# Kernel optimization log

Measured on AMD Instinct MI355X. Metric: run time of the kernel, lower is better.

## Reference

```python
import jax, jax.numpy as jnp
import numpy as np
from jax.scipy.linalg import solve_triangular

B, T, HID = 1, 2048, 2048
HK, DK = 16, 96
HV, DV = 16, 192
KDIM, VDIM = HK * DK, HV * DV
KCONV = 4
CHUNK = 64
EPS = 1e-6


def setup_inputs():
    key = jax.random.key(0)
    ks = jax.random.split(key, 16)
    s = 0.02
    return {
        "hidden_states": jax.random.normal(ks[0], (B, T, HID), jnp.float32),
        "Wq": jax.random.normal(ks[1], (HID, KDIM), jnp.float32) * s,
        "Wk": jax.random.normal(ks[2], (HID, KDIM), jnp.float32) * s,
        "Wv": jax.random.normal(ks[3], (HID, VDIM), jnp.float32) * s,
        "Wb": jax.random.normal(ks[4], (HID, HV), jnp.float32) * s,
        "Wa": jax.random.normal(ks[5], (HID, HV), jnp.float32) * s,
        "Wg": jax.random.normal(ks[6], (HID, VDIM), jnp.float32) * s,
        "Wo": jax.random.normal(ks[7], (VDIM, HID), jnp.float32) * s,
        "conv_q": jax.random.normal(ks[8], (KDIM, KCONV), jnp.float32) * 0.5,
        "conv_k": jax.random.normal(ks[9], (KDIM, KCONV), jnp.float32) * 0.5,
        "conv_v": jax.random.normal(ks[10], (VDIM, KCONV), jnp.float32) * 0.5,
        "A_log": jnp.log(jax.random.uniform(ks[11], (HV,), jnp.float32, 1.0, 16.0)),
        "dt_bias": jax.random.uniform(ks[12], (HV,), jnp.float32, 0.0, 1.0),
        "norm_weight": jnp.ones((DV,), jnp.float32),
    }


def short_conv_silu(x, w):
    # x: [B,T,C], w: [C,K]; causal depthwise conv (left pad K-1) then SiLU
    K = w.shape[-1]
    xp = jnp.pad(x, ((0, 0), (K - 1, 0), (0, 0)))
    y = sum(xp[:, j:j + x.shape[1], :] * w[:, j] for j in range(K))
    return jax.nn.silu(y)


def l2norm(x):
    return x * jax.lax.rsqrt(jnp.sum(x * x, axis=-1, keepdims=True) + EPS)


def chunk_gated_delta_rule(q, k, v, g, beta):
    # q,k: [B,T,H,dk]; v: [B,T,H,dv]; g,beta: [B,T,H]. Chunked parallel scan (WY form).
    Bb, Tt, H, dk = q.shape
    dv = v.shape[-1]
    N = Tt // CHUNK
    q = l2norm(q) * (dk ** -0.5)
    k = l2norm(k)
    chunk = lambda x: x.transpose(0, 2, 1, 3).reshape(Bb, H, N, CHUNK, x.shape[-1])
    qc, kc, vc = chunk(q), chunk(k), chunk(v)
    gc = jnp.cumsum(g.transpose(0, 2, 1).reshape(Bb, H, N, CHUNK), axis=-1)
    bc = beta.transpose(0, 2, 1).reshape(Bb, H, N, CHUNK)

    m_inc = jnp.tril(jnp.ones((CHUNK, CHUNK), bool))
    m_str = jnp.tril(jnp.ones((CHUNK, CHUNK), bool), -1)
    diff = gc[..., :, None] - gc[..., None, :]
    D = jnp.exp(jnp.where(m_inc, diff, 0.0)) * m_inc  # [B,H,N,C,C] intra-chunk decay

    kb = kc * bc[..., None]
    A = -jnp.einsum('bhnik,bhnjk->bhnij', kb, kc) * D * m_str
    eye = jnp.eye(CHUNK, dtype=q.dtype)
    # UT transform: Tm = (I - A)^{-1}, A strictly lower triangular
    Tm = solve_triangular(eye - A, jnp.broadcast_to(eye, A.shape), lower=True, unit_diagonal=True)
    u = Tm @ (vc * bc[..., None])                   # [B,H,N,C,dv]
    w = Tm @ (kb * jnp.exp(gc)[..., None])          # [B,H,N,C,dk]
    g_last = gc[..., -1]                            # [B,H,N]

    def step(S, inp):
        q_i, k_i, u_i, w_i, g_i, D_i, gl = inp
        v_new = u_i - w_i @ S                       # [B,H,C,dv]
        attn = jnp.einsum('bhik,bhjk->bhij', q_i, k_i) * D_i
        o_i = (q_i * jnp.exp(g_i)[..., None]) @ S + attn @ v_new
        k_dec = k_i * jnp.exp(gl[..., None] - g_i)[..., None]
        S = S * jnp.exp(gl)[..., None, None] + jnp.einsum('bhck,bhcv->bhkv', k_dec, v_new)
        return S, o_i

    mv = lambda x: jnp.moveaxis(x, 2, 0)
    S0 = jnp.zeros((Bb, H, dk, dv), q.dtype)
    _, o = jax.lax.scan(step, S0, (mv(qc), mv(kc), mv(u), mv(w), mv(gc), mv(D), mv(g_last)))
    o = jnp.moveaxis(o, 0, 2).reshape(Bb, H, Tt, dv)
    return o.transpose(0, 2, 1, 3)                  # [B,T,H,dv]


def reference(hidden_states, Wq, Wk, Wv, Wb, Wa, Wg, Wo, conv_q, conv_k, conv_v, A_log, dt_bias, norm_weight):
    q = short_conv_silu(hidden_states @ Wq, conv_q).reshape(B, T, HK, DK)
    k = short_conv_silu(hidden_states @ Wk, conv_k).reshape(B, T, HK, DK)
    v = short_conv_silu(hidden_states @ Wv, conv_v).reshape(B, T, HV, DV)
    beta = jax.nn.sigmoid(hidden_states @ Wb) * 2.0          # allow_neg_eigval -> beta in [0,2]
    g = -jnp.exp(A_log) * jax.nn.softplus(hidden_states @ Wa + dt_bias)  # log decay, [B,T,HV]
    o = chunk_gated_delta_rule(q, k, v, g, beta)             # [B,T,HV,DV]
    gate = (hidden_states @ Wg).reshape(B, T, HV, DV)
    o = o * jax.nn.silu(gate)                                # gated RMSNorm (gate, then norm)
    o = o * jax.lax.rsqrt(jnp.mean(o * o, axis=-1, keepdims=True) + EPS) * norm_weight
    return o.reshape(B, T, VDIM) @ Wo
```

## Files before the change

### kernel.cpp

```cpp
#include <hip/hip_runtime.h>
#include <math.h>

#define T_LEN 2048
#define HIDN  2048
#define HKN   16
#define DKN   96
#define HVN   16
#define DVN   192
#define KDIMN 1536
#define VDIMN 3072
#define QKVD  6144
#define CHUNKN 64
#define NCHUNK 32
#define EPSF 1e-6f
#define TN_STRIDE 10240
#define WQG_ST 6656
#define AT_ST  4608
#define CT_ST  18432
#define S_ST   19968
#define U_ST   12288

typedef __attribute__((ext_vector_type(8))) short short8;
typedef __attribute__((ext_vector_type(4))) float f32x4;

__device__ __forceinline__ unsigned short f2bf(float f) {
    unsigned int u = __float_as_uint(f);
    unsigned int r = (u + 0x7FFFu + ((u >> 16) & 1u)) >> 16;
    return (unsigned short)r;
}
__device__ __forceinline__ float bf2f(unsigned short u) {
    return __uint_as_float(((unsigned int)u) << 16);
}
__device__ __forceinline__ float siluf(float x) { return x / (1.f + expf(-x)); }

__device__ __forceinline__ void gld_lds16(const void* g, void* l) {
    __builtin_amdgcn_global_load_lds((const __attribute__((address_space(1))) unsigned int*)g,
                                     (__attribute__((address_space(3))) unsigned int*)l, 16, 0, 0);
}

__global__ void prep_weights(const float* __restrict__ Wq, const float* __restrict__ Wk,
                             const float* __restrict__ Wv, const float* __restrict__ Wg,
                             const float* __restrict__ Wo,
                             unsigned short* __restrict__ WallT, unsigned short* __restrict__ WoT) {
    __shared__ float tile[64][65];
    int bid = blockIdx.x;
    const float* W; unsigned short* Wt; int K, N, l;
    if (bid < 768)       { W = Wq; Wt = WallT;                          K = 2048; N = 1536; l = bid; }
    else if (bid < 1536) { W = Wk; Wt = WallT + (size_t)1536 * 2048;    K = 2048; N = 1536; l = bid - 768; }
    else if (bid < 3072) { W = Wv; Wt = WallT + (size_t)3072 * 2048;    K = 2048; N = 3072; l = bid - 1536; }
    else if (bid < 4608) { W = Wg; Wt = WallT + (size_t)6144 * 2048;    K = 2048; N = 3072; l = bid - 3072; }
    else                 { W = Wo; Wt = WoT;                            K = 3072; N = 2048; l = bid - 4608; }
    int nbx = N >> 6;
    int n0 = (l % nbx) * 64, k0 = (l / nbx) * 64;
    int tx = threadIdx.x, ty = threadIdx.y;
    for (int r = ty; r < 64; r += 4) tile[r][tx] = W[(size_t)(k0 + r) * N + n0 + tx];
    __syncthreads();
    for (int r = ty; r < 64; r += 4) Wt[(size_t)(n0 + r) * K + k0 + tx] = f2bf(tile[tx][r]);
}

__global__ __launch_bounds__(256) void gemm_bt2(const unsigned short* __restrict__ A,
                                                const unsigned short* __restrict__ Bt,
                                                float* __restrict__ C1, int ld1, int nblk1,
                                                unsigned short* __restrict__ C2, int ld2,
                                                int M, int K) {
    __shared__ __align__(16) unsigned short As[2][128 * 32];
    __shared__ __align__(16) unsigned short Bs[2][128 * 32];
    int tid = threadIdx.x;
    int wave = tid >> 6, lane = tid & 63;
    int bm = blockIdx.y, bn = blockIdx.x;
    f32x4 acc[4][4] = {};
    int wr = wave >> 1, wc = wave & 1;
    int rstage = wave * 32 + (lane >> 2);
    int cstage = (lane & 3) * 8;
    const size_t a_row0 = (size_t)bm * 128;
    const size_t b_row0 = (size_t)bn * 128;
    const unsigned short* gaBase = A + (a_row0 + rstage) * (size_t)K + cstage;
    const unsigned short* gbBase = Bt + (b_row0 + rstage) * (size_t)K + cstage;
    int row_a[4], row_b[4];
#pragma unroll
    for (int i = 0; i < 4; ++i) {
        row_a[i] = wr * 64 + i * 16 + (lane & 15);
        row_b[i] = wc * 64 + i * 16 + (lane & 15);
    }
    int koff = (lane >> 4) * 8;
    int niter = K >> 5;
    {
        unsigned short* ab = &As[0][wave * 1024];
        unsigned short* bb = &Bs[0][wave * 1024];
        gld_lds16(gaBase, ab);
        gld_lds16(gaBase + (size_t)16 * K, ab + 512);
        gld_lds16(gbBase, bb);
        gld_lds16(gbBase + (size_t)16 * K, bb + 512);
    }
    __syncthreads();
    for (int i = 0; i < niter; ++i) {
        int cur = i & 1;
        if (i + 1 < niter) {
            int k0 = (i + 1) * 32;
            unsigned short* ab = &As[cur ^ 1][wave * 1024];
            unsigned short* bb = &Bs[cur ^ 1][wave * 1024];
            gld_lds16(gaBase + k0, ab);
            gld_lds16(gaBase + k0 + (size_t)16 * K, ab + 512);
            gld_lds16(gbBase + k0, bb);
            gld_lds16(gbBase + k0 + (size_t)16 * K, bb + 512);
        }
        short8 af[4], bfr[4];
#pragma unroll
        for (int mi = 0; mi < 4; ++mi) af[mi] = *(const short8*)&As[cur][row_a[mi] * 32 + koff];
#pragma unroll
        for (int ni = 0; ni < 4; ++ni) bfr[ni] = *(const short8*)&Bs[cur][row_b[ni] * 32 + koff];
#pragma unroll
        for (int mi = 0; mi < 4; ++mi)
#pragma unroll
            for (int ni = 0; ni < 4; ++ni)
                acc[mi][ni] = __builtin_amdgcn_mfma_f32_16x16x32_bf16(af[mi], bfr[ni], acc[mi][ni], 0, 0, 0);
        __syncthreads();
    }
    if (bn < nblk1) {
        int colb = bn * 128;
#pragma unroll
        for (int mi = 0; mi < 4; ++mi) {
            int rbase = bm * 128 + wr * 64 + mi * 16 + (lane >> 4) * 4;
#pragma unroll
            for (int ni = 0; ni < 4; ++ni) {
                int col = colb + wc * 64 + ni * 16 + (lane & 15);
#pragma unroll
                for (int j = 0; j < 4; ++j)
                    C1[(size_t)(rbase + j) * ld1 + col] = acc[mi][ni][j];
            }
        }
    } else {
        int colb = (bn - nblk1) * 128;
#pragma unroll
        for (int mi = 0; mi < 4; ++mi) {
            int rbase = bm * 128 + wr * 64 + mi * 16 + (lane >> 4) * 4;
#pragma unroll
            for (int ni = 0; ni < 4; ++ni) {
                int col = colb + wc * 64 + ni * 16 + (lane & 15);
#pragma unroll
                for (int j = 0; j < 4; ++j)
                    C2[(size_t)(rbase + j) * ld2 + col] = f2bf(acc[mi][ni][j]);
            }
        }
    }
}

__global__ __launch_bounds__(256) void gemm_btk(const unsigned short* __restrict__ A,
                                                const unsigned short* __restrict__ Bt,
                                                float* __restrict__ C, float* __restrict__ Cp,
                                                int M, int N, int K) {
    __shared__ __align__(16) unsigned short As[2][128 * 32];
    __shared__ __align__(16) unsigned short Bs[2][128 * 32];
    int tid = threadIdx.x;
    int wave = tid >> 6, lane = tid & 63;
    int bm = blockIdx.y, bn = blockIdx.x, kz = blockIdx.z;
    int kchunk = K / 3;
    int kbeg = kz * kchunk;
    f32x4 acc[4][4] = {};
    int wr = wave >> 1, wc = wave & 1;
    int rstage = wave * 32 + (lane >> 2);
    int cstage = (lane & 3) * 8;
    const size_t a_row0 = (size_t)bm * 128;
    const size_t b_row0 = (size_t)bn * 128;
    const unsigned short* gaBase = A + (a_row0 + rstage) * (size_t)K + kbeg + cstage;
    const unsigned short* gbBase = Bt + (b_row0 + rstage) * (size_t)K + kbeg + cstage;
    int row_a[4], row_b[4];
#pragma unroll
    for (int i = 0; i < 4; ++i) {
        row_a[i] = wr * 64 + i * 16 + (lane & 15);
        row_b[i] = wc * 64 + i * 16 + (lane & 15);
    }
    int koff = (lane >> 4) * 8;
    int niter = kchunk >> 5;
    {
        unsigned short* ab = &As[0][wave * 1024];
        unsigned short* bb = &Bs[0][wave * 1024];
        gld_lds16(gaBase, ab);
        gld_lds16(gaBase + (size_t)16 * K, ab + 512);
        gld_lds16(gbBase, bb);
        gld_lds16(gbBase + (size_t)16 * K, bb + 512);
    }
    __syncthreads();
    for (int i = 0; i < niter; ++i) {
        int cur = i & 1;
        if (i + 1 < niter) {
            int k0 = (i + 1) * 32;
            unsigned short* ab = &As[cur ^ 1][wave * 1024];
            unsigned short* bb = &Bs[cur ^ 1][wave * 1024];
            gld_lds16(gaBase + k0, ab);
            gld_lds16(gaBase + k0 + (size_t)16 * K, ab + 512);
            gld_lds16(gbBase + k0, bb);
            gld_lds16(gbBase + k0 + (size_t)16 * K, bb + 512);
        }
        short8 af[4], bfr[4];
#pragma unroll
        for (int mi = 0; mi < 4; ++mi) af[mi] = *(const short8*)&As[cur][row_a[mi] * 32 + koff];
#pragma unroll
        for (int ni = 0; ni < 4; ++ni) bfr[ni] = *(const short8*)&Bs[cur][row_b[ni] * 32 + koff];
#pragma unroll
        for (int mi = 0; mi < 4; ++mi)
#pragma unroll
            for (int ni = 0; ni < 4; ++ni)
                acc[mi][ni] = __builtin_amdgcn_mfma_f32_16x16x32_bf16(af[mi], bfr[ni], acc[mi][ni], 0, 0, 0);
        __syncthreads();
    }
    float* Cout = (kz == 0) ? C : (Cp + (size_t)(kz - 1) * M * N);
#pragma unroll
    for (int mi = 0; mi < 4; ++mi) {
        int rbase = bm * 128 + wr * 64 + mi * 16 + (lane >> 4) * 4;
#pragma unroll
        for (int ni = 0; ni < 4; ++ni) {
            int col = bn * 128 + wc * 64 + ni * 16 + (lane & 15);
#pragma unroll
            for (int j = 0; j < 4; ++j)
                Cout[(size_t)(rbase + j) * N + col] = acc[mi][ni][j];
        }
    }
}

__global__ void addk(float* __restrict__ out, const float* __restrict__ p, int n) {
    int i = (blockIdx.x * blockDim.x + threadIdx.x) * 4;
    if (i >= n) return;
    float4 a = *(const float4*)(out + i);
    float4 b = *(const float4*)(p + i);
    float4 c = *(const float4*)(p + n + i);
    a.x += b.x + c.x; a.y += b.y + c.y; a.z += b.z + c.z; a.w += b.w + c.w;
    *(float4*)(out + i) = a;
}

__global__ __launch_bounds__(256) void beta_g(const float* __restrict__ X,
                                              const float* __restrict__ Wb, const float* __restrict__ Wa,
                                              const float* __restrict__ A_log, const float* __restrict__ dtb,
                                              float* __restrict__ bvec, float* __restrict__ gvec,
                                              unsigned short* __restrict__ Xbf) {
    int t = blockIdx.x;
    int tid = threadIdx.x;
    int cg = tid & 7, ks = tid >> 3;
    int wave = tid >> 6, lane = tid & 63;
    const float* xr = X + (size_t)t * HIDN;
    const float* Wsel = (cg < 4) ? Wb : Wa;
    int cc = (cg & 3) * 4;
    float ax = 0.f, ay = 0.f, az = 0.f, aw = 0.f;
#pragma unroll 4
    for (int i = 0; i < 16; ++i) {
        int k = (ks + 32 * i) * 4;
        float4 xv = *(const float4*)(xr + k);
        if (cg == 0) {
            ushort4 xo;
            xo.x = f2bf(xv.x); xo.y = f2bf(xv.y); xo.z = f2bf(xv.z); xo.w = f2bf(xv.w);
            *(ushort4*)(Xbf + (size_t)t * HIDN + k) = xo;
        }
        float4 w0 = *(const float4*)(Wsel + (size_t)(k + 0) * 16 + cc);
        float4 w1 = *(const float4*)(Wsel + (size_t)(k + 1) * 16 + cc);
        float4 w2 = *(const float4*)(Wsel + (size_t)(k + 2) * 16 + cc);
        float4 w3 = *(const float4*)(Wsel + (size_t)(k + 3) * 16 + cc);
        ax += xv.x * w0.x + xv.y * w1.x + xv.z * w2.x + xv.w * w3.x;
        ay += xv.x * w0.y + xv.y * w1.y + xv.z * w2.y + xv.w * w3.y;
        az += xv.x * w0.z + xv.y * w1.z + xv.z * w2.z + xv.w * w3.z;
        aw += xv.x * w0.w + xv.y * w1.w + xv.z * w2.w + xv.w * w3.w;
    }
#pragma unroll
    for (int off = 8; off <= 32; off <<= 1) {
        ax += __shfl_xor(ax, off, 64);
        ay += __shfl_xor(ay, off, 64);
        az += __shfl_xor(az, off, 64);
        aw += __shfl_xor(aw, off, 64);
    }
    __shared__ float red[4][8][4];
    if ((lane >> 3) == 0) {
        red[wave][cg][0] = ax; red[wave][cg][1] = ay;
        red[wave][cg][2] = az; red[wave][cg][3] = aw;
    }
    __syncthreads();
    if (tid < 8) {
        float tot[4];
#pragma unroll
        for (int j = 0; j < 4; ++j)
            tot[j] = red[0][tid][j] + red[1][tid][j] + red[2][tid][j] + red[3][tid][j];
        int c0 = (tid & 3) * 4;
        if (tid < 4) {
#pragma unroll
            for (int j = 0; j < 4; ++j)
                bvec[(size_t)t * 16 + c0 + j] = 2.f / (1.f + expf(-tot[j]));
        } else {
#pragma unroll
            for (int j = 0; j < 4; ++j) {
                float a = tot[j] + dtb[c0 + j];
                float sp = (a > 20.f) ? a : log1pf(expf(a));
                gvec[(size_t)t * 16 + c0 + j] = -expf(A_log[c0 + j]) * sp;
            }
        }
    }
}

__global__ __launch_bounds__(256) void phase1_mfma(
    const float* __restrict__ Cqkv,
    const float* __restrict__ cq, const float* __restrict__ ck, const float* __restrict__ cv,
    const float* __restrict__ gvec, const float* __restrict__ bvec,
    float* __restrict__ u_ws, unsigned short* __restrict__ w_bf,
    unsigned short* __restrict__ qg_bf, unsigned short* __restrict__ at_bf,
    unsigned short* __restrict__ Ct, unsigned short* __restrict__ Tn) {
    int n = blockIdx.x, h = blockIdx.y;
    int t0 = n * CHUNKN;
    int tid = threadIdx.x;
    int wave = tid >> 6, lane = tid & 63;
    size_t base = (size_t)(h * NCHUNK + n);

    __shared__ __align__(16) char LB1[139776];
    unsigned short* QKb  = (unsigned short*)(LB1 + 0);
    unsigned short* Pb   = (unsigned short*)(LB1 + 26624);
    unsigned short* RHSw = (unsigned short*)(LB1 + 39936);
    unsigned short* RHSv = (unsigned short*)(LB1 + 53760);
    unsigned short* Ab   = (unsigned short*)(LB1 + 81408);
    unsigned short* Atb  = (unsigned short*)(LB1 + 94720);
    unsigned short* Ptb  = (unsigned short*)(LB1 + 108032);
    float*          Pf   = (float*)(LB1 + 121344);
    unsigned short* kdT  = (unsigned short*)(LB1 + 81408);
    unsigned short* wT   = (unsigned short*)(LB1 + 95232);
    unsigned short* uT   = (unsigned short*)(LB1 + 109056);
    float* gr_s = (float*)(LB1 + 138752);
    float* gc_s = gr_s + 64;
    float* be_s = gc_s + 64;
    float* egc  = be_s + 64;
    __shared__ __align__(16) float cwS[384 * 4];

    for (int f = tid; f < 384; f += 256) {
        const float* src = (f < 96)  ? (cq + (size_t)(h * 96 + f) * 4)
                         : (f < 192) ? (ck + (size_t)(h * 96 + f - 96) * 4)
                                     : (cv + (size_t)(h * 192 + f - 192) * 4);
        *(float4*)&cwS[f * 4] = *(const float4*)src;
    }
    if (tid < 64) {
        gr_s[tid] = gvec[(size_t)(t0 + tid) * HVN + h];
        be_s[tid] = bvec[(size_t)(t0 + tid) * HVN + h];
    }
    __syncthreads();
    if (tid < 64) {
        float sacc = 0.f;
        for (int j = 0; j <= tid; ++j) sacc += gr_s[j];
        gc_s[tid] = sacc;
    }
    __syncthreads();
    float gl = gc_s[63];
    if (tid < 64) egc[tid] = expf(gl - gc_s[tid]);

    int r = tid >> 2, sub = tid & 3;
    int trow = t0 + r;
    {
        int gc0 = 1536 + h * DKN + sub * 24;
        int lc0 = 96 + sub * 24;
        float kreg[24];
        float ss = 0.f;
#pragma unroll
        for (int i = 0; i < 6; ++i) {
            float4 x0 = (trow >= 3) ? *(const float4*)(Cqkv + (size_t)(trow - 3) * QKVD + gc0 + i * 4) : make_float4(0, 0, 0, 0);
            float4 x1 = (trow >= 2) ? *(const float4*)(Cqkv + (size_t)(trow - 2) * QKVD + gc0 + i * 4) : make_float4(0, 0, 0, 0);
            float4 x2 = (trow >= 1) ? *(const float4*)(Cqkv + (size_t)(trow - 1) * QKVD + gc0 + i * 4) : make_float4(0, 0, 0, 0);
            float4 x3 = *(const float4*)(Cqkv + (size_t)trow * QKVD + gc0 + i * 4);
#pragma unroll
            for (int c = 0; c < 4; ++c) {
                float4 w = *(const float4*)&cwS[(lc0 + i * 4 + c) * 4];
                float xv = ((const float*)&x0)[c] * w.x + ((const float*)&x1)[c] * w.y
                         + ((const float*)&x2)[c] * w.z + ((const float*)&x3)[c] * w.w;
                xv = siluf(xv);
                kreg[i * 4 + c] = xv;
                ss += xv * xv;
            }
        }
        ss += __shfl_xor(ss, 1, 64);
        ss += __shfl_xor(ss, 2, 64);
        float nrm = rsqrtf(ss + EPSF);
        float ebg = be_s[r] * expf(gc_s[r]);
#pragma unroll
        for (int i = 0; i < 24; ++i) {
            float kn = kreg[i] * nrm;
            QKb[r * 104 + sub * 24 + i] = f2bf(kn);
            RHSw[(sub * 24 + i) * 72 + r] = f2bf(kn * ebg);
        }
    }
    {
        int gc0 = h * DKN + sub * 24;
        int lc0 = sub * 24;
        float qreg[24];
        float ss = 0.f;
#pragma unroll
        for (int i = 0; i < 6; ++i) {
            float4 x0 = (trow >= 3) ? *(const float4*)(Cqkv + (size_t)(trow - 3) * QKVD + gc0 + i * 4) : make_float4(0, 0, 0, 0);
            float4 x1 = (trow >= 2) ? *(const float4*)(Cqkv + (size_t)(trow - 2) * QKVD + gc0 + i * 4) : make_float4(0, 0, 0, 0);
            float4 x2 = (trow >= 1) ? *(const float4*)(Cqkv + (size_t)(trow - 1) * QKVD + gc0 + i * 4) : make_float4(0, 0, 0, 0);
            float4 x3 = *(const float4*)(Cqkv + (size_t)trow * QKVD + gc0 + i * 4);
#pragma unroll
            for (int c = 0; c < 4; ++c) {
                float4 w = *(const float4*)&cwS[(lc0 + i * 4 + c) * 4];
                float xv = ((const float*)&x0)[c] * w.x + ((const float*)&x1)[c] * w.y
                         + ((const float*)&x2)[c] * w.z + ((const float*)&x3)[c] * w.w;
                xv = siluf(xv);
                qreg[i * 4 + c] = xv;
                ss += xv * xv;
            }
        }
        ss += __shfl_xor(ss, 1, 64);
        ss += __shfl_xor(ss, 2, 64);
        float nrm = rsqrtf(ss + EPSF) * 0.10206207261596577f;
        float eg = expf(gc_s[r]);
        unsigned short* qgp = qg_bf + base * WQG_ST + r * 104 + sub * 24;
#pragma unroll
        for (int i = 0; i < 24; ++i) {
            float qn = qreg[i] * nrm;
            QKb[(64 + r) * 104 + sub * 24 + i] = f2bf(qn);
            qgp[i] = f2bf(qn * eg);
        }
    }
    {
        int gc0 = 3072 + h * DVN + sub * 48;
        int lc0 = 192 + sub * 48;
        float ber = be_s[r];
#pragma unroll
        for (int i = 0; i < 12; ++i) {
            float4 x0 = (trow >= 3) ? *(const float4*)(Cqkv + (size_t)(trow - 3) * QKVD + gc0 + i * 4) : make_float4(0, 0, 0, 0);
            float4 x1 = (trow >= 2) ? *(const float4*)(Cqkv + (size_t)(trow - 2) * QKVD + gc0 + i * 4) : make_float4(0, 0, 0, 0);
            float4 x2 = (trow >= 1) ? *(const float4*)(Cqkv + (size_t)(trow - 1) * QKVD + gc0 + i * 4) : make_float4(0, 0, 0, 0);
            float4 x3 = *(const float4*)(Cqkv + (size_t)trow * QKVD + gc0 + i * 4);
#pragma unroll
            for (int c = 0; c < 4; ++c) {
                float4 w = *(const float4*)&cwS[(lc0 + i * 4 + c) * 4];
                float xv = ((const float*)&x0)[c] * w.x + ((const float*)&x1)[c] * w.y
                         + ((const float*)&x2)[c] * w.z + ((const float*)&x3)[c] * w.w;
                RHSv[(sub * 48 + i * 4 + c) * 72 + r] = f2bf(siluf(xv) * ber);
            }
        }
    }
    __syncthreads();

    {
        f32x4 acc1[2][4] = {};
#pragma unroll
        for (int ks = 0; ks < 3; ++ks) {
            int ko = ks * 32 + (lane >> 4) * 8;
            short8 af[2], bfv[4];
#pragma unroll
            for (int rt2 = 0; rt2 < 2; ++rt2)
                af[rt2] = *(const short8*)&QKb[(wave * 32 + rt2 * 16 + (lane & 15)) * 104 + ko];
#pragma unroll
            for (int ct = 0; ct < 4; ++ct)
                bfv[ct] = *(const short8*)&QKb[(ct * 16 + (lane & 15)) * 104 + ko];
#pragma unroll
            for (int rt2 = 0; rt2 < 2; ++rt2)
#pragma unroll
                for (int ct = 0; ct < 4; ++ct)
                    acc1[rt2][ct] = __builtin_amdgcn_mfma_f32_16x16x32_bf16(af[rt2], bfv[ct], acc1[rt2][ct], 0, 0, 0);
        }
#pragma unroll
        for (int rt2 = 0; rt2 < 2; ++rt2)
#pragma unroll
            for (int ct = 0; ct < 4; ++ct)
#pragma unroll
                for (int j = 0; j < 4; ++j) {
                    int rr = wave * 32 + rt2 * 16 + (lane >> 4) * 4 + j;
                    int cc = ct * 16 + (lane & 15);
                    float val = acc1[rt2][ct][j];
                    if (rr < 64) {
                        float av = (rr > cc) ? -be_s[rr] * expf(gc_s[rr] - gc_s[cc]) * val : 0.f;
                        unsigned short ab = f2bf(av);
                        Ab[rr * 104 + cc] = ab;
                        Atb[cc * 104 + rr] = ab;
                        float pv = (rr == cc) ? 1.f : av;
                        Pf[rr * 68 + cc] = pv;
                        unsigned short pb = f2bf(pv);
                        Pb[rr * 104 + cc] = pb;
                        Ptb[cc * 104 + rr] = pb;
                    } else {
                        int ar = rr - 64;
                        float av = (ar >= cc) ? expf(gc_s[ar] - gc_s[cc]) * val : 0.f;
                        at_bf[base * AT_ST + ar * 72 + cc] = f2bf(av);
                    }
                }
    }
    __syncthreads();

#pragma unroll 1
    for (int lev = 0; lev < 5; ++lev) {
        f32x4 d[4] = {};
#pragma unroll
        for (int ks = 0; ks < 2; ++ks) {
            int ko = ks * 32 + (lane >> 4) * 8;
            short8 a0 = *(const short8*)&Ab[(wave * 16 + (lane & 15)) * 104 + ko];
#pragma unroll
            for (int ct = 0; ct < 4; ++ct) {
                short8 b0 = *(const short8*)&Atb[(ct * 16 + (lane & 15)) * 104 + ko];
                d[ct] = __builtin_amdgcn_mfma_f32_16x16x32_bf16(a0, b0, d[ct], 0, 0, 0);
            }
        }
        __syncthreads();
#pragma unroll
        for (int ct = 0; ct < 4; ++ct)
#pragma unroll
            for (int j = 0; j < 4; ++j) {
                int rr = wave * 16 + (lane >> 4) * 4 + j;
                int cc = ct * 16 + (lane & 15);
                unsigned short hb = f2bf(d[ct][j]);
                Ab[rr * 104 + cc] = hb;
                Atb[cc * 104 + rr] = hb;
            }
        __syncthreads();
        f32x4 e[4];
#pragma unroll
        for (int ct = 0; ct < 4; ++ct)
#pragma unroll
            for (int j = 0; j < 4; ++j)
                e[ct][j] = Pf[(wave * 16 + (lane >> 4) * 4 + j) * 68 + ct * 16 + (lane & 15)];
#pragma unroll
        for (int ks = 0; ks < 2; ++ks) {
            int ko = ks * 32 + (lane >> 4) * 8;
            short8 a0 = *(const short8*)&Ab[(wave * 16 + (lane & 15)) * 104 + ko];
#pragma unroll
            for (int ct = 0; ct < 4; ++ct) {
                short8 b0 = *(const short8*)&Ptb[(ct * 16 + (lane & 15)) * 104 + ko];
                e[ct] = __builtin_amdgcn_mfma_f32_16x16x32_bf16(a0, b0, e[ct], 0, 0, 0);
            }
        }
        __syncthreads();
#pragma unroll
        for (int ct = 0; ct < 4; ++ct)
#pragma unroll
            for (int j = 0; j < 4; ++j) {
                int rr = wave * 16 + (lane >> 4) * 4 + j;
                int cc = ct * 16 + (lane & 15);
                float pv = e[ct][j];
                Pf[rr * 68 + cc] = pv;
                unsigned short pb = f2bf(pv);
                Pb[rr * 104 + cc] = pb;
                Ptb[cc * 104 + rr] = pb;
            }
        __syncthreads();
    }
    for (int f = tid; f < 6144; f += 256) {
        int d = f >> 6, tt = f & 63;
        kdT[d * 72 + tt] = f2bf(bf2f(QKb[tt * 104 + d]) * egc[tt]);
    }

#pragma unroll 1
    for (int i = 0; i < 18; ++i) {
        int id = wave * 18 + i;
        int rt = id & 3, ct = id >> 2;
        f32x4 o4 = {};
#pragma unroll
        for (int ks = 0; ks < 2; ++ks) {
            int ko = ks * 32 + (lane >> 4) * 8;
            short8 a0 = *(const short8*)&Pb[(rt * 16 + (lane & 15)) * 104 + ko];
            short8 b0 = (ct < 12)
                ? *(const short8*)&RHSv[(ct * 16 + (lane & 15)) * 72 + ko]
                : *(const short8*)&RHSw[((ct - 12) * 16 + (lane & 15)) * 72 + ko];
            o4 = __builtin_amdgcn_mfma_f32_16x16x32_bf16(a0, b0, o4, 0, 0, 0);
        }
#pragma unroll
        for (int j = 0; j < 4; ++j) {
            int rr = rt * 16 + (lane >> 4) * 4 + j;
            int nn = ct * 16 + (lane & 15);
            if (ct < 12) {
                u_ws[base * U_ST + rr * 192 + nn] = o4[j];
                uT[nn * 72 + rr] = f2bf(o4[j]);
            } else {
                w_bf[base * WQG_ST + rr * 104 + (nn - 192)] = f2bf(-o4[j]);
                wT[(nn - 192) * 72 + rr] = f2bf(o4[j]);
            }
        }
    }
    __syncthreads();

    float eglv = expf(gl);
#pragma unroll 1
    for (int q = 0; q < 27; ++q) {
        int id = wave * 27 + q;
        f32x4 acc = {};
        if (id < 36) {
            int jt = id / 6, kt = id % 6;
#pragma unroll
            for (int ks = 0; ks < 2; ++ks) {
                int ko = ks * 32 + (lane >> 4) * 8;
                short8 a0 = *(const short8*)&kdT[(jt * 16 + (lane & 15)) * 72 + ko];
                short8 b0 = *(const short8*)&wT[(kt * 16 + (lane & 15)) * 72 + ko];
                acc = __builtin_amdgcn_mfma_f32_16x16x32_bf16(a0, b0, acc, 0, 0, 0);
            }
#pragma unroll
            for (int rr = 0; rr < 4; ++rr) {
                int j = jt * 16 + (lane >> 4) * 4 + rr;
                int k = kt * 16 + (lane & 15);
                float val = -acc[rr];
                if (j == k) val += eglv;
                Tn[base * TN_STRIDE + j * 104 + k] = f2bf(val);
            }
        } else {
            int cid = id - 36;
            int it = cid / 6, jt = cid % 6;
#pragma unroll
            for (int ks = 0; ks < 2; ++ks) {
                int ko = ks * 32 + (lane >> 4) * 8;
                short8 a0 = *(const short8*)&uT[(it * 16 + (lane & 15)) * 72 + ko];
                short8 b0 = *(const short8*)&kdT[(jt * 16 + (lane & 15)) * 72 + ko];
                acc = __builtin_amdgcn_mfma_f32_16x16x32_bf16(a0, b0, acc, 0, 0, 0);
            }
#pragma unroll
            for (int rr = 0; rr < 4; ++rr)
                Ct[base * CT_ST + (size_t)(it * 16 + (lane >> 4) * 4 + rr) * 96 + jt * 16 + (lane & 15)] = f2bf(acc[rr]);
        }
    }
}

__global__ __launch_bounds__(128) void mscan(const unsigned short* __restrict__ Ct,
                                             const unsigned short* __restrict__ Tn,
                                             unsigned short* __restrict__ s_bf) {
    int rg = blockIdx.x, h = blockIdx.y;
    int tid = threadIdx.x, wave = tid >> 6, lane = tid & 63;
    __shared__ __align__(16) unsigned short St[48 * 104];
    __shared__ __align__(16) unsigned short TnB[2][TN_STRIDE];
// ... 208 lines not shown
        for (int m = 0; m < 48; ++m) {
            int i = qq * 48 + m;
            float x = oF[i * 68 + jj];
            float g = bf2f(gp[m]);
            float xv = x * siluf(g);
            oF[i * 68 + jj] = xv;
            ss += xv * xv;
        }
        ssq[jj * 4 + qq] = ss;
    }
    __syncthreads();
    if (tid < 64) {
        float tot = ssq[tid * 4] + ssq[tid * 4 + 1] + ssq[tid * 4 + 2] + ssq[tid * 4 + 3];
        rno[tid] = rsqrtf(tot * (1.f / 192.f) + EPSF);
    }
    __syncthreads();
    {
        float rr2 = rno[jj];
        unsigned short* op = obf + (size_t)(t0 + jj) * VDIMN + h * DVN + qq * 48;
#pragma unroll 4
        for (int m = 0; m < 48; ++m) {
            int i = qq * 48 + m;
            op[m] = f2bf(oF[i * 68 + jj] * rr2 * nw[i]);
        }
    }
}

extern "C" void kernel_launch(void* const* d_in, const int* in_sizes, int n_in,
                              void* d_out, int out_size, void* d_ws, size_t ws_size,
                              hipStream_t stream) {
    (void)in_sizes; (void)n_in; (void)out_size;
    const float* X    = (const float*)d_in[0];
    const float* Wq   = (const float*)d_in[1];
    const float* Wk   = (const float*)d_in[2];
    const float* Wv   = (const float*)d_in[3];
    const float* Wb   = (const float*)d_in[4];
    const float* Wa   = (const float*)d_in[5];
    const float* Wg   = (const float*)d_in[6];
    const float* Wo   = (const float*)d_in[7];
    const float* cq   = (const float*)d_in[8];
    const float* ck   = (const float*)d_in[9];
    const float* cv   = (const float*)d_in[10];
    const float* Alog = (const float*)d_in[11];
    const float* dtb  = (const float*)d_in[12];
    const float* nw   = (const float*)d_in[13];

    const size_t OFF_XBF   = 0;
    const size_t OFF_WALLT = 8388608;
    const size_t OFF_WOT   = 46137344;
    const size_t OFF_CQKV  = 58720256;
    const size_t OFF_CGATE = 109051904;
    const size_t OFF_CT    = 134217728;
    const size_t OFF_TN    = OFF_CT + 37748736;
    const size_t OFF_GVEC  = 184549376;
    const size_t OFF_BVEC  = 184680448;
    const size_t OFF_U     = 184819712;
    const size_t OFF_W     = 209985536;
    const size_t OFF_QG    = 222568448;
    const size_t OFF_AT    = OFF_XBF;
    const size_t OFF_S     = OFF_CQKV;
    const size_t OFF_OBF   = OFF_WALLT + 25165824;
    const size_t OFF_OPART = OFF_CQKV;
    const size_t NEEDED    = 235151360;
    if (ws_size < NEEDED) return;

    char* ws = (char*)d_ws;
    unsigned short* Xbf   = (unsigned short*)(ws + OFF_XBF);
    unsigned short* WallT = (unsigned short*)(ws + OFF_WALLT);
    unsigned short* WoT   = (unsigned short*)(ws + OFF_WOT);
    float* Cqkv  = (float*)(ws + OFF_CQKV);
    unsigned short* Cgate = (unsigned short*)(ws + OFF_CGATE);
    float* gvec  = (float*)(ws + OFF_GVEC);
    float* bvec  = (float*)(ws + OFF_BVEC);
    float* u_ws  = (float*)(ws + OFF_U);
    unsigned short* w_bf  = (unsigned short*)(ws + OFF_W);
    unsigned short* qg_bf = (unsigned short*)(ws + OFF_QG);
    unsigned short* at_bf = (unsigned short*)(ws + OFF_AT);
    unsigned short* Ct    = (unsigned short*)(ws + OFF_CT);
    unsigned short* Tn    = (unsigned short*)(ws + OFF_TN);
    unsigned short* s_bf  = (unsigned short*)(ws + OFF_S);
    unsigned short* obf   = (unsigned short*)(ws + OFF_OBF);
    float* opart = (float*)(ws + OFF_OPART);

    beta_g<<<T_LEN, 256, 0, stream>>>(X, Wb, Wa, Alog, dtb, bvec, gvec, Xbf);
    prep_weights<<<6144, dim3(64, 4), 0, stream>>>(Wq, Wk, Wv, Wg, Wo, WallT, WoT);

    gemm_bt2<<<dim3(9216 / 128, 2048 / 128), 256, 0, stream>>>(Xbf, WallT,
                                                               Cqkv, QKVD, QKVD / 128,
                                                               Cgate, VDIMN, 2048, 2048);

    phase1_mfma<<<dim3(NCHUNK, HVN), 256, 0, stream>>>(Cqkv, cq, ck, cv, gvec, bvec,
                                                       u_ws, w_bf, qg_bf, at_bf, Ct, Tn);
    mscan<<<dim3(4, HVN), 128, 0, stream>>>(Ct, Tn, s_bf);
    phase2b_mfma<<<dim3(NCHUNK, HVN), 256, 0, stream>>>(s_bf, w_bf, qg_bf, at_bf, u_ws,
                                                        Cgate, nw, obf);

    gemm_btk<<<dim3(2048 / 128, 2048 / 128, 3), 256, 0, stream>>>(obf, WoT, (float*)d_out, opart,
                                                                  2048, 2048, 3072);
    addk<<<4096, 256, 0, stream>>>((float*)d_out, opart, 2048 * 2048);
}
```

Baseline: 402.7 us.

## Deepen GEMM K-tiles with swizzled LDS, merge prep kernels, restructure inverse doubling

```diff
diff --git a/kernel.cpp b/kernel.cpp
--- a/kernel.cpp
+++ b/kernel.cpp
@@ -38,24 +38,106 @@
                                      (__attribute__((address_space(3))) unsigned int*)l, 16, 0, 0);
 }
 
-__global__ void prep_weights(const float* __restrict__ Wq, const float* __restrict__ Wk,
-                             const float* __restrict__ Wv, const float* __restrict__ Wg,
-                             const float* __restrict__ Wo,
-                             unsigned short* __restrict__ WallT, unsigned short* __restrict__ WoT) {
+__device__ __forceinline__ void stage_tile64(const unsigned short* __restrict__ G,
+                                             size_t row0, int K, int kt,
+                                             unsigned short* lds, int wave, int lane) {
+#pragma unroll
+    for (int q = 0; q < 4; ++q) {
+        int c = q * 4 + wave;
+        int row = c * 8 + (lane >> 3);
+        int col = ((lane & 7) ^ (lane >> 3)) * 8;
+        gld_lds16(G + (row0 + row) * (size_t)K + kt + col, (char*)lds + c * 1024);
+    }
+}
+__device__ __forceinline__ short8 lds_read_swz(const unsigned short* lds, int row, int kbyte) {
+    return *(const short8*)((const char*)lds + row * 128 + (kbyte ^ ((row & 7) << 4)));
+}
+
+__global__ __launch_bounds__(256) void prep_all(
+    const float* __restrict__ X,
+    const float* __restrict__ Wb, const float* __restrict__ Wa,
+    const float* __restrict__ A_log, const float* __restrict__ dtb,
+    float* __restrict__ bvec, float* __restrict__ gvec, unsigned short* __restrict__ Xbf,
+    const float* __restrict__ Wq, const float* __restrict__ Wk,
+    const float* __restrict__ Wv, const float* __restrict__ Wg,
+    const float* __restrict__ Wo,
+    unsigned short* __restrict__ WallT, unsigned short* __restrict__ WoT) {
     __shared__ float tile[64][65];
+    __shared__ float red[4][8][4];
     int bid = blockIdx.x;
-    const float* W; unsigned short* Wt; int K, N, l;
-    if (bid < 768)       { W = Wq; Wt = WallT;                          K = 2048; N = 1536; l = bid; }
-    else if (bid < 1536) { W = Wk; Wt = WallT + (size_t)1536 * 2048;    K = 2048; N = 1536; l = bid - 768; }
-    else if (bid < 3072) { W = Wv; Wt = WallT + (size_t)3072 * 2048;    K = 2048; N = 3072; l = bid - 1536; }
-    else if (bid < 4608) { W = Wg; Wt = WallT + (size_t)6144 * 2048;    K = 2048; N = 3072; l = bid - 3072; }
-    else                 { W = Wo; Wt = WoT;                            K = 3072; N = 2048; l = bid - 4608; }
-    int nbx = N >> 6;
-    int n0 = (l % nbx) * 64, k0 = (l / nbx) * 64;
-    int tx = threadIdx.x, ty = threadIdx.y;
-    for (int r = ty; r < 64; r += 4) tile[r][tx] = W[(size_t)(k0 + r) * N + n0 + tx];
-    __syncthreads();
-    for (int r = ty; r < 64; r += 4) Wt[(size_t)(n0 + r) * K + k0 + tx] = f2bf(tile[tx][r]);
+    int tid = threadIdx.x;
+    if (bid < 2048) {
+        int t = bid;
+        int cg = tid & 7, ks = tid >> 3;
+        int wave = tid >> 6, lane = tid & 63;
+        const float* xr = X + (size_t)t * HIDN;
+        const float* Wsel = (cg < 4) ? Wb : Wa;
+        int cc = (cg & 3) * 4;
+        float ax = 0.f, ay = 0.f, az = 0.f, aw = 0.f;
+#pragma unroll 4
+        for (int i = 0; i < 16; ++i) {
+            int k = (ks + 32 * i) * 4;
+            float4 xv = *(const float4*)(xr + k);
+            if (cg == 0) {
+                ushort4 xo;
+                xo.x = f2bf(xv.x); xo.y = f2bf(xv.y); xo.z = f2bf(xv.z); xo.w = f2bf(xv.w);
+                *(ushort4*)(Xbf + (size_t)t * HIDN + k) = xo;
+            }
+            float4 w0 = *(const float4*)(Wsel + (size_t)(k + 0) * 16 + cc);
+            float4 w1 = *(const float4*)(Wsel + (size_t)(k + 1) * 16 + cc);
+            float4 w2 = *(const float4*)(Wsel + (size_t)(k + 2) * 16 + cc);
+            float4 w3 = *(const float4*)(Wsel + (size_t)(k + 3) * 16 + cc);
+            ax += xv.x * w0.x + xv.y * w1.x + xv.z * w2.x + xv.w * w3.x;
+            ay += xv.x * w0.y + xv.y * w1.y + xv.z * w2.y + xv.w * w3.y;
+            az += xv.x * w0.z + xv.y * w1.z + xv.z * w2.z + xv.w * w3.z;
+            aw += xv.x * w0.w + xv.y * w1.w + xv.z * w2.w + xv.w * w3.w;
+        }
+#pragma unroll
+        for (int off = 8; off <= 32; off <<= 1) {
+            ax += __shfl_xor(ax, off, 64);
+            ay += __shfl_xor(ay, off, 64);
+            az += __shfl_xor(az, off, 64);
+            aw += __shfl_xor(aw, off, 64);
+        }
+        if ((lane >> 3) == 0) {
+            red[wave][cg][0] = ax; red[wave][cg][1] = ay;
+            red[wave][cg][2] = az; red[wave][cg][3] = aw;
+        }
+        __syncthreads();
+        if (tid < 8) {
+            float tot[4];
+#pragma unroll
+            for (int j = 0; j < 4; ++j)
+                tot[j] = red[0][tid][j] + red[1][tid][j] + red[2][tid][j] + red[3][tid][j];
+            int c0 = (tid & 3) * 4;
+            if (tid < 4) {
+#pragma unroll
+                for (int j = 0; j < 4; ++j)
+                    bvec[(size_t)t * 16 + c0 + j] = 2.f / (1.f + expf(-tot[j]));
+            } else {
+#pragma unroll
+                for (int j = 0; j < 4; ++j) {
+                    float a = tot[j] + dtb[c0 + j];
+                    float sp = (a > 20.f) ? a : log1pf(expf(a));
+                    gvec[(size_t)t * 16 + c0 + j] = -expf(A_log[c0 + j]) * sp;
+                }
+            }
+        }
+    } else {
+        int b2 = bid - 2048;
+        const float* W; unsigned short* Wt; int K, N, l;
+        if (b2 < 768)       { W = Wq; Wt = WallT;                       K = 2048; N = 1536; l = b2; }
+        else if (b2 < 1536) { W = Wk; Wt = WallT + (size_t)1536 * 2048; K = 2048; N = 1536; l = b2 - 768; }
+        else if (b2 < 3072) { W = Wv; Wt = WallT + (size_t)3072 * 2048; K = 2048; N = 3072; l = b2 - 1536; }
+        else if (b2 < 4608) { W = Wg; Wt = WallT + (size_t)6144 * 2048; K = 2048; N = 3072; l = b2 - 3072; }
+        else                { W = Wo; Wt = WoT;                         K = 3072; N = 2048; l = b2 - 4608; }
+        int nbx = N >> 6;
+        int n0 = (l % nbx) * 64, k0 = (l / nbx) * 64;
+        int tx = tid & 63, ty = tid >> 6;
+        for (int r = ty; r < 64; r += 4) tile[r][tx] = W[(size_t)(k0 + r) * N + n0 + tx];
+        __syncthreads();
+        for (int r = ty; r < 64; r += 4) Wt[(size_t)(n0 + r) * K + k0 + tx] = f2bf(tile[tx][r]);
+    }
 }
 
 __global__ __launch_bounds__(256) void gemm_bt2(const unsigned short* __restrict__ A,
@@ -63,57 +145,45 @@
                                                 float* __restrict__ C1, int ld1, int nblk1,
                                                 unsigned short* __restrict__ C2, int ld2,
                                                 int M, int K) {
-    __shared__ __align__(16) unsigned short As[2][128 * 32];
-    __shared__ __align__(16) unsigned short Bs[2][128 * 32];
+    __shared__ __align__(16) unsigned short As[2][128 * 64];
+    __shared__ __align__(16) unsigned short Bs[2][128 * 64];
     int tid = threadIdx.x;
     int wave = tid >> 6, lane = tid & 63;
     int bm = blockIdx.y, bn = blockIdx.x;
     f32x4 acc[4][4] = {};
     int wr = wave >> 1, wc = wave & 1;
-    int rstage = wave * 32 + (lane >> 2);
-    int cstage = (lane & 3) * 8;
     const size_t a_row0 = (size_t)bm * 128;
     const size_t b_row0 = (size_t)bn * 128;
-    const unsigned short* gaBase = A + (a_row0 + rstage) * (size_t)K + cstage;
-    const unsigned short* gbBase = Bt + (b_row0 + rstage) * (size_t)K + cstage;
     int row_a[4], row_b[4];
 #pragma unroll
     for (int i = 0; i < 4; ++i) {
         row_a[i] = wr * 64 + i * 16 + (lane & 15);
         row_b[i] = wc * 64 + i * 16 + (lane & 15);
     }
-    int koff = (lane >> 4) * 8;
-    int niter = K >> 5;
-    {
-        unsigned short* ab = &As[0][wave * 1024];
-        unsigned short* bb = &Bs[0][wave * 1024];
-        gld_lds16(gaBase, ab);
-        gld_lds16(gaBase + (size_t)16 * K, ab + 512);
-        gld_lds16(gbBase, bb);
-        gld_lds16(gbBase + (size_t)16 * K, bb + 512);
-    }
+    int niter = K >> 6;
+    stage_tile64(A, a_row0, K, 0, &As[0][0], wave, lane);
+    stage_tile64(Bt, b_row0, K, 0, &Bs[0][0], wave, lane);
     __syncthreads();
     for (int i = 0; i < niter; ++i) {
         int cur = i & 1;
         if (i + 1 < niter) {
-            int k0 = (i + 1) * 32;
-            unsigned short* ab = &As[cur ^ 1][wave * 1024];
-            unsigned short* bb = &Bs[cur ^ 1][wave * 1024];
-            gld_lds16(gaBase + k0, ab);
-            gld_lds16(gaBase + k0 + (size_t)16 * K, ab + 512);
-            gld_lds16(gbBase + k0, bb);
-            gld_lds16(gbBase + k0 + (size_t)16 * K, bb + 512);
-        }
-        short8 af[4], bfr[4];
-#pragma unroll
-        for (int mi = 0; mi < 4; ++mi) af[mi] = *(const short8*)&As[cur][row_a[mi] * 32 + koff];
-#pragma unroll
-        for (int ni = 0; ni < 4; ++ni) bfr[ni] = *(const short8*)&Bs[cur][row_b[ni] * 32 + koff];
-#pragma unroll
-        for (int mi = 0; mi < 4; ++mi)
-#pragma unroll
-            for (int ni = 0; ni < 4; ++ni)
-                acc[mi][ni] = __builtin_amdgcn_mfma_f32_16x16x32_bf16(af[mi], bfr[ni], acc[mi][ni], 0, 0, 0);
+            stage_tile64(A, a_row0, K, (i + 1) * 64, &As[cur ^ 1][0], wave, lane);
+            stage_tile64(Bt, b_row0, K, (i + 1) * 64, &Bs[cur ^ 1][0], wave, lane);
+        }
+#pragma unroll
+        for (int ks2 = 0; ks2 < 2; ++ks2) {
+            int kb = ks2 * 64 + (lane >> 4) * 16;
+            short8 af[4], bfr[4];
+#pragma unroll
+            for (int mi = 0; mi < 4; ++mi) af[mi] = lds_read_swz(&As[cur][0], row_a[mi], kb);
+#pragma unroll
+            for (int ni = 0; ni < 4; ++ni) bfr[ni] = lds_read_swz(&Bs[cur][0], row_b[ni], kb);
+#pragma unroll
+            for (int mi = 0; mi < 4; ++mi)
+#pragma unroll
+                for (int ni = 0; ni < 4; ++ni)
+                    acc[mi][ni] = __builtin_amdgcn_mfma_f32_16x16x32_bf16(af[mi], bfr[ni], acc[mi][ni], 0, 0, 0);
+        }
         __syncthreads();
     }
     if (bn < nblk1) {
@@ -149,8 +219,8 @@
                                                 const unsigned short* __restrict__ Bt,
                                                 float* __restrict__ C, float* __restrict__ Cp,
                                                 int M, int N, int K) {
-    __shared__ __align__(16) unsigned short As[2][128 * 32];
-    __shared__ __align__(16) unsigned short Bs[2][128 * 32];
+    __shared__ __align__(16) unsigned short As[2][128 * 64];
+    __shared__ __align__(16) unsigned short Bs[2][128 * 64];
     int tid = threadIdx.x;
     int wave = tid >> 6, lane = tid & 63;
     int bm = blockIdx.y, bn = blockIdx.x, kz = blockIdx.z;
@@ -158,50 +228,38 @@
     int kbeg = kz * kchunk;
     f32x4 acc[4][4] = {};
     int wr = wave >> 1, wc = wave & 1;
-    int rstage = wave * 32 + (lane >> 2);
-    int cstage = (lane & 3) * 8;
     const size_t a_row0 = (size_t)bm * 128;
     const size_t b_row0 = (size_t)bn * 128;
-    const unsigned short* gaBase = A + (a_row0 + rstage) * (size_t)K + kbeg + cstage;
-    const unsigned short* gbBase = Bt + (b_row0 + rstage) * (size_t)K + kbeg + cstage;
     int row_a[4], row_b[4];
 #pragma unroll
     for (int i = 0; i < 4; ++i) {
         row_a[i] = wr * 64 + i * 16 + (lane & 15);
         row_b[i] = wc * 64 + i * 16 + (lane & 15);
     }
-    int koff = (lane >> 4) * 8;
-    int niter = kchunk >> 5;
-    {
-        unsigned short* ab = &As[0][wave * 1024];
-        unsigned short* bb = &Bs[0][wave * 1024];
-        gld_lds16(gaBase, ab);
-        gld_lds16(gaBase + (size_t)16 * K, ab + 512);
-        gld_lds16(gbBase, bb);
-        gld_lds16(gbBase + (size_t)16 * K, bb + 512);
-    }
+    int niter = kchunk >> 6;
+    stage_tile64(A, a_row0, K, kbeg, &As[0][0], wave, lane);
+    stage_tile64(Bt, b_row0, K, kbeg, &Bs[0][0], wave, lane);
     __syncthreads();
     for (int i = 0; i < niter; ++i) {
         int cur = i & 1;
         if (i + 1 < niter) {
-            int k0 = (i + 1) * 32;
-            unsigned short* ab = &As[cur ^ 1][wave * 1024];
-            unsigned short* bb = &Bs[cur ^ 1][wave * 1024];
-            gld_lds16(gaBase + k0, ab);
-            gld_lds16(gaBase + k0 + (size_t)16 * K, ab + 512);
-            gld_lds16(gbBase + k0, bb);
-            gld_lds16(gbBase + k0 + (size_t)16 * K, bb + 512);
-        }
-        short8 af[4], bfr[4];
-#pragma unroll
-        for (int mi = 0; mi < 4; ++mi) af[mi] = *(const short8*)&As[cur][row_a[mi] * 32 + koff];
-#pragma unroll
-        for (int ni = 0; ni < 4; ++ni) bfr[ni] = *(const short8*)&Bs[cur][row_b[ni] * 32 + koff];
-#pragma unroll
-        for (int mi = 0; mi < 4; ++mi)
-#pragma unroll
-            for (int ni = 0; ni < 4; ++ni)
-                acc[mi][ni] = __builtin_amdgcn_mfma_f32_16x16x32_bf16(af[mi], bfr[ni], acc[mi][ni], 0, 0, 0);
+            stage_tile64(A, a_row0, K, kbeg + (i + 1) * 64, &As[cur ^ 1][0], wave, lane);
+            stage_tile64(Bt, b_row0, K, kbeg + (i + 1) * 64, &Bs[cur ^ 1][0], wave, lane);
+        }
+#pragma unroll
+        for (int ks2 = 0; ks2 < 2; ++ks2) {
+            int kb = ks2 * 64 + (lane >> 4) * 16;
+            short8 af[4], bfr[4];
+#pragma unroll
+            for (int mi = 0; mi < 4; ++mi) af[mi] = lds_read_swz(&As[cur][0], row_a[mi], kb);
+#pragma unroll
+            for (int ni = 0; ni < 4; ++ni) bfr[ni] = lds_read_swz(&Bs[cur][0], row_b[ni], kb);
+#pragma unroll
+            for (int mi = 0; mi < 4; ++mi)
+#pragma unroll
+                for (int ni = 0; ni < 4; ++ni)
+                    acc[mi][ni] = __builtin_amdgcn_mfma_f32_16x16x32_bf16(af[mi], bfr[ni], acc[mi][ni], 0, 0, 0);
+        }
         __syncthreads();
     }
     float* Cout = (kz == 0) ? C : (Cp + (size_t)(kz - 1) * M * N);
@@ -226,71 +284,6 @@
     float4 c = *(const float4*)(p + n + i);
     a.x += b.x + c.x; a.y += b.y + c.y; a.z += b.z + c.z; a.w += b.w + c.w;
     *(float4*)(out + i) = a;
-}
-
-__global__ __launch_bounds__(256) void beta_g(const float* __restrict__ X,
-                                              const float* __restrict__ Wb, const float* __restrict__ Wa,
-                                              const float* __restrict__ A_log, const float* __restrict__ dtb,
-                                              float* __restrict__ bvec, float* __restrict__ gvec,
-                                              unsigned short* __restrict__ Xbf) {
-    int t = blockIdx.x;
-    int tid = threadIdx.x;
-    int cg = tid & 7, ks = tid >> 3;
-    int wave = tid >> 6, lane = tid & 63;
-    const float* xr = X + (size_t)t * HIDN;
-    const float* Wsel = (cg < 4) ? Wb : Wa;
-    int cc = (cg & 3) * 4;
-    float ax = 0.f, ay = 0.f, az = 0.f, aw = 0.f;
-#pragma unroll 4
-    for (int i = 0; i < 16; ++i) {
-        int k = (ks + 32 * i) * 4;
-        float4 xv = *(const float4*)(xr + k);
-        if (cg == 0) {
-            ushort4 xo;
-            xo.x = f2bf(xv.x); xo.y = f2bf(xv.y); xo.z = f2bf(xv.z); xo.w = f2bf(xv.w);
-            *(ushort4*)(Xbf + (size_t)t * HIDN + k) = xo;
-        }
-        float4 w0 = *(const float4*)(Wsel + (size_t)(k + 0) * 16 + cc);
-        float4 w1 = *(const float4*)(Wsel + (size_t)(k + 1) * 16 + cc);
-        float4 w2 = *(const float4*)(Wsel + (size_t)(k + 2) * 16 + cc);
-        float4 w3 = *(const float4*)(Wsel + (size_t)(k + 3) * 16 + cc);
-        ax += xv.x * w0.x + xv.y * w1.x + xv.z * w2.x + xv.w * w3.x;
-        ay += xv.x * w0.y + xv.y * w1.y + xv.z * w2.y + xv.w * w3.y;
-        az += xv.x * w0.z + xv.y * w1.z + xv.z * w2.z + xv.w * w3.z;
-        aw += xv.x * w0.w + xv.y * w1.w + xv.z * w2.w + xv.w * w3.w;
-    }
-#pragma unroll
-    for (int off = 8; off <= 32; off <<= 1) {
-        ax += __shfl_xor(ax, off, 64);
-        ay += __shfl_xor(ay, off, 64);
-        az += __shfl_xor(az, off, 64);
-        aw += __shfl_xor(aw, off, 64);
-    }
-    __shared__ float red[4][8][4];
-    if ((lane >> 3) == 0) {
-        red[wave][cg][0] = ax; red[wave][cg][1] = ay;
-        red[wave][cg][2] = az; red[wave][cg][3] = aw;
-    }
-    __syncthreads();
-    if (tid < 8) {
-        float tot[4];
-#pragma unroll
-        for (int j = 0; j < 4; ++j)
-            tot[j] = red[0][tid][j] + red[1][tid][j] + red[2][tid][j] + red[3][tid][j];
-        int c0 = (tid & 3) * 4;
-        if (tid < 4) {
-#pragma unroll
-            for (int j = 0; j < 4; ++j)
-                bvec[(size_t)t * 16 + c0 + j] = 2.f / (1.f + expf(-tot[j]));
-        } else {
-#pragma unroll
-            for (int j = 0; j < 4; ++j) {
-                float a = tot[j] + dtb[c0 + j];
-                float sp = (a > 20.f) ? a : log1pf(expf(a));
-                gvec[(size_t)t * 16 + c0 + j] = -expf(A_log[c0 + j]) * sp;
-            }
-        }
-    }
 }
 
 __global__ __launch_bounds__(256) void phase1_mfma(
@@ -313,7 +306,6 @@
     unsigned short* RHSv = (unsigned short*)(LB1 + 53760);
     unsigned short* Ab   = (unsigned short*)(LB1 + 81408);
     unsigned short* Atb  = (unsigned short*)(LB1 + 94720);
-    unsigned short* Ptb  = (unsigned short*)(LB1 + 108032);
     float*          Pf   = (float*)(LB1 + 121344);
     unsigned short* kdT  = (unsigned short*)(LB1 + 81408);
     unsigned short* wT   = (unsigned short*)(LB1 + 95232);
@@ -464,11 +456,9 @@
                         unsigned short ab = f2bf(av);
                         Ab[rr * 104 + cc] = ab;
                         Atb[cc * 104 + rr] = ab;
-                        float pv = (rr == cc) ? 1.f : av;
+                        float pv = (rr == cc) ? 1.f : 0.f;
                         Pf[rr * 68 + cc] = pv;
-                        unsigned short pb = f2bf(pv);
-                        Pb[rr * 104 + cc] = pb;
-                        Ptb[cc * 104 + rr] = pb;
+                        Pb[rr * 104 + cc] = f2bf(pv);
                     } else {
                         int ar = rr - 64;
                         float av = (ar >= cc) ? expf(gc_s[ar] - gc_s[cc]) * val : 0.f;
@@ -479,16 +469,24 @@
     __syncthreads();
 
 #pragma unroll 1
-    for (int lev = 0; lev < 5; ++lev) {
+    for (int lev = 0; lev < 6; ++lev) {
         f32x4 d[4] = {};
+        f32x4 e[4];
+#pragma unroll
+        for (int ct = 0; ct < 4; ++ct)
+#pragma unroll
+            for (int j = 0; j < 4; ++j)
+                e[ct][j] = Pf[(wave * 16 + (lane >> 4) * 4 + j) * 68 + ct * 16 + (lane & 15)];
 #pragma unroll
         for (int ks = 0; ks < 2; ++ks) {
             int ko = ks * 32 + (lane >> 4) * 8;
-            short8 a0 = *(const short8*)&Ab[(wave * 16 + (lane & 15)) * 104 + ko];
+            short8 aA = *(const short8*)&Ab[(wave * 16 + (lane & 15)) * 104 + ko];
+            short8 aP = *(const short8*)&Pb[(wave * 16 + (lane & 15)) * 104 + ko];
 #pragma unroll
             for (int ct = 0; ct < 4; ++ct) {
-                short8 b0 = *(const short8*)&Atb[(ct * 16 + (lane & 15)) * 104 + ko];
-                d[ct] = __builtin_amdgcn_mfma_f32_16x16x32_bf16(a0, b0, d[ct], 0, 0, 0);
+                short8 bAt = *(const short8*)&Atb[(ct * 16 + (lane & 15)) * 104 + ko];
+                if (lev < 5) d[ct] = __builtin_amdgcn_mfma_f32_16x16x32_bf16(aA, bAt, d[ct], 0, 0, 0);
+                e[ct] = __builtin_amdgcn_mfma_f32_16x16x32_bf16(aP, bAt, e[ct], 0, 0, 0);
             }
         }
         __syncthreads();
@@ -498,39 +496,14 @@
             for (int j = 0; j < 4; ++j) {
                 int rr = wave * 16 + (lane >> 4) * 4 + j;
                 int cc = ct * 16 + (lane & 15);
-                unsigned short hb = f2bf(d[ct][j]);
-                Ab[rr * 104 + cc] = hb;
-                Atb[cc * 104 + rr] = hb;
-            }
-        __syncthreads();
-        f32x4 e[4];
-#pragma unroll
-        for (int ct = 0; ct < 4; ++ct)
-#pragma unroll
-            for (int j = 0; j < 4; ++j)
-                e[ct][j] = Pf[(wave * 16 + (lane >> 4) * 4 + j) * 68 + ct * 16 + (lane & 15)];
-#pragma unroll
-        for (int ks = 0; ks < 2; ++ks) {
-            int ko = ks * 32 + (lane >> 4) * 8;
-            short8 a0 = *(const short8*)&Ab[(wave * 16 + (lane & 15)) * 104 + ko];
-#pragma unroll
-            for (int ct = 0; ct < 4; ++ct) {
-                short8 b0 = *(const short8*)&Ptb[(ct * 16 + (lane & 15)) * 104 + ko];
-                e[ct] = __builtin_amdgcn_mfma_f32_16x16x32_bf16(a0, b0, e[ct], 0, 0, 0);
-            }
-        }
-        __syncthreads();
-#pragma unroll
-        for (int ct = 0; ct < 4; ++ct)
-#pragma unroll
-            for (int j = 0; j < 4; ++j) {
-                int rr = wave * 16 + (lane >> 4) * 4 + j;
-                int cc = ct * 16 + (lane & 15);
+                if (lev < 5) {
+                    unsigned short hb = f2bf(d[ct][j]);
+                    Ab[rr * 104 + cc] = hb;
+                    Atb[cc * 104 + rr] = hb;
+                }
                 float pv = e[ct][j];
                 Pf[rr * 68 + cc] = pv;
-                unsigned short pb = f2bf(pv);
-                Pb[rr * 104 + cc] = pb;
-                Ptb[cc * 104 + rr] = pb;
+                Pb[rr * 104 + cc] = f2bf(pv);
             }
         __syncthreads();
     }
@@ -905,8 +878,8 @@
     unsigned short* obf   = (unsigned short*)(ws + OFF_OBF);
     float* opart = (float*)(ws + OFF_OPART);
 
-    beta_g<<<T_LEN, 256, 0, stream>>>(X, Wb, Wa, Alog, dtb, bvec, gvec, Xbf);
-    prep_weights<<<6144, dim3(64, 4), 0, stream>>>(Wq, Wk, Wv, Wg, Wo, WallT, WoT);
+    prep_all<<<8192, 256, 0, stream>>>(X, Wb, Wa, Alog, dtb, bvec, gvec, Xbf,
+                                       Wq, Wk, Wv, Wg, Wo, WallT, WoT);
 
     gemm_bt2<<<dim3(9216 / 128, 2048 / 128), 256, 0, stream>>>(Xbf, WallT,
                                                                Cqkv, QKVD, QKVD / 128,
```

Result: no change. 406.0 us (+0.8%).
